# Kernel tuning notes

Measured on AMD Instinct MI355X. Metric: run time of the kernel, lower is better.

## Reference

```python
import jax, jax.numpy as jnp
import numpy as np

N_ENT = 500000
N_REL = 64
HID = 256
EMB = 128
E = 400000


def setup_inputs() -> dict:
    key = jax.random.key(0)
    k0, k1, k2, k3, k4 = jax.random.split(key, 5)
    s_in = 1.0 / np.sqrt(N_ENT + N_REL)
    s_h = 1.0 / np.sqrt(HID)
    return {
        "edge_index": jax.random.randint(k0, (2, E), 0, N_ENT),
        "edge_attr": jax.random.normal(k1, (E, N_REL), dtype=jnp.float32),
        "W1": jax.random.normal(k2, (N_ENT + N_REL, HID), dtype=jnp.float32) * s_in,
        "b1": jnp.zeros((HID,), dtype=jnp.float32),
        "W2": jax.random.normal(k3, (HID, HID), dtype=jnp.float32) * s_h,
        "b2": jnp.zeros((HID,), dtype=jnp.float32),
        "W3": jax.random.normal(k4, (HID, EMB), dtype=jnp.float32) * s_h,
        "b3": jnp.zeros((EMB,), dtype=jnp.float32),
    }


def reference(edge_index, edge_attr, W1, b1, W2, b2, W3, b3):
    # one_hot(edge_index, N_ENT) @ W1_ent is exactly a row gather from W1_ent.
    W1_ent = W1[:N_ENT]          # [N_ENT, HID]
    W1_rel = W1[N_ENT:]          # [N_REL, HID]
    rel_proj = edge_attr @ W1_rel            # [E, HID], shared by source/target
    h = W1_ent[edge_index] + rel_proj[None] + b1   # [2, E, HID]
    h = jax.nn.relu(h)
    h = jax.nn.relu(h @ W2 + b2)             # [2, E, HID]
    edge_emb = h @ W3 + b3                   # [2, E, EMB]
    return edge_emb
```

## Files before the change

kernel.cpp:

```cpp
#include <hip/hip_runtime.h>

#define N_ENT 500000
#define E_NUM 400000

typedef __attribute__((ext_vector_type(8))) short short8;
typedef __attribute__((ext_vector_type(4))) float f32x4;

static __device__ __forceinline__ unsigned short f2bf(float f) {
    unsigned u = __float_as_uint(f);
    u += 0x7fffu + ((u >> 16) & 1u);
    return (unsigned short)(u >> 16);
}
static __device__ __forceinline__ float bf2f(unsigned short s) {
    return __uint_as_float(((unsigned)s) << 16);
}

__global__ void pack_b_kernel(const float* __restrict__ src,
                              unsigned short* __restrict__ dst, int K, int N) {
    int p = blockIdx.x * blockDim.x + threadIdx.x;
    if (p >= K * N) return;
    int j = p & 7;
    int l = (p >> 3) & 63;
    int f = p >> 9;
    int nfr = N >> 4;
    int nb = f % nfr;
    int kb = f / nfr;
    int k = kb * 32 + ((l >> 4) << 3) + j;
    int n = nb * 16 + (l & 15);
    dst[p] = f2bf(src[(size_t)k * N + n]);
}

__device__ __forceinline__ int lds_off(int row, int colb) {
    return ((row << 9) + colb) ^ ((row & 7) << 4);
}

__global__ __launch_bounds__(256, 4) void fused2(
    const int* __restrict__ ei, const float* __restrict__ attr,
    const float* __restrict__ W1, const float* __restrict__ b1,
    const float* __restrict__ b2, const float* __restrict__ b3,
    const unsigned short* __restrict__ w1rp,
    const unsigned short* __restrict__ w2p,
    const unsigned short* __restrict__ w3p,
    float* __restrict__ out)
{
    __shared__ char hb[64 * 512];

    const int tid = threadIdx.x;
    const int l = tid & 63;
    const int wv = tid >> 6;
    const int lr = l & 15;
    const int lg = l >> 4;
    const int r0 = wv << 4;
    const int myrow = l >> 4;
    const int mycol = l & 15;

    const int bid = blockIdx.x;
    const int d = bid >= 6250 ? 1 : 0;
    const int e0 = (d ? bid - 6250 : bid) << 6;

    int ids[4];
    #pragma unroll
    for (int q = 0; q < 4; ++q)
        ids[q] = ei[d * E_NUM + e0 + r0 + (q << 2) + myrow];

    f32x4 g[4][4];
    #pragma unroll
    for (int q = 0; q < 4; ++q) {
        const float* gp = W1 + (size_t)ids[q] * 256 + (mycol << 2);
        #pragma unroll
        for (int k = 0; k < 4; ++k)
            g[q][k] = *(const f32x4*)(gp + (k << 6));
    }

    const float* ap = attr + (size_t)(e0 + r0 + lr) * 64 + (lg << 3);
    f32x4 ax[2][2];
    #pragma unroll
    for (int kb = 0; kb < 2; ++kb) {
        ax[kb][0] = *(const f32x4*)(ap + (kb << 5));
        ax[kb][1] = *(const f32x4*)(ap + (kb << 5) + 4);
    }

    #pragma unroll
    for (int q = 0; q < 4; ++q) {
        int row = r0 + (q << 2) + myrow;
        #pragma unroll
        for (int k = 0; k < 4; ++k) {
            unsigned lo = ((unsigned)f2bf(g[q][k][1]) << 16) | f2bf(g[q][k][0]);
            unsigned hi = ((unsigned)f2bf(g[q][k][3]) << 16) | f2bf(g[q][k][2]);
            int a = lds_off(row, (k << 7) + (mycol << 3));
            *(unsigned*)(hb + a) = lo;
            *(unsigned*)(hb + a + 4) = hi;
        }
    }

    const f32x4 zero = {0.f, 0.f, 0.f, 0.f};
    f32x4 acc[16];
    #pragma unroll
    for (int i = 0; i < 16; ++i) acc[i] = zero;
    #pragma unroll
    for (int kb = 0; kb < 2; ++kb) {
        short8 af;
        #pragma unroll
        for (int j = 0; j < 4; ++j) {
            af[j] = (short)f2bf(ax[kb][0][j]);
            af[j + 4] = (short)f2bf(ax[kb][1][j]);
        }
        #pragma unroll
        for (int cf = 0; cf < 16; ++cf)
            acc[cf] = __builtin_amdgcn_mfma_f32_16x16x32_bf16(
                af, ((const short8*)w1rp)[(size_t)(kb * 16 + cf) * 64 + l],
                acc[cf], 0, 0, 0);
    }

    #pragma unroll
    for (int reg = 0; reg < 4; ++reg) {
        int row = r0 + (lg << 2) + reg;
        #pragma unroll
        for (int cf = 0; cf < 16; ++cf) {
            int col = (cf << 4) + lr;
            int a = lds_off(row, col << 1);
            float v = acc[cf][reg] + bf2f(*(unsigned short*)(hb + a)) + b1[col];
            *(unsigned short*)(hb + a) = f2bf(fmaxf(v, 0.f));
        }
    }
    __syncthreads();

    f32x4 acc2[4][4];
    #pragma unroll
    for (int i = 0; i < 4; ++i)
        #pragma unroll
        for (int j = 0; j < 4; ++j) acc2[i][j] = zero;

    #pragma unroll 2
    for (int kb = 0; kb < 8; ++kb) {
        short8 a[4];
        #pragma unroll
        for (int mr = 0; mr < 4; ++mr)
            a[mr] = *(const short8*)(hb +
                lds_off(mr * 16 + lr, ((kb << 5) + (lg << 3)) << 1));
        #pragma unroll
        for (int mr = 0; mr < 4; ++mr)
            #pragma unroll
            for (int nf = 0; nf < 4; ++nf)
                acc2[mr][nf] = __builtin_amdgcn_mfma_f32_16x16x32_bf16(
                    a[mr],
                    ((const short8*)w2p)[(size_t)(kb * 16 + (wv << 2) + nf) * 64 + l],
                    acc2[mr][nf], 0, 0, 0);
    }
    __syncthreads();

    #pragma unroll
    for (int mr = 0; mr < 4; ++mr)
        #pragma unroll
        for (int reg = 0; reg < 4; ++reg) {
            int row = mr * 16 + (lg << 2) + reg;
            #pragma unroll
            for (int nf = 0; nf < 4; ++nf) {
                int col = (wv << 6) + (nf << 4) + lr;
                float v = fmaxf(acc2[mr][nf][reg] + b2[col], 0.f);
                *(unsigned short*)(hb + lds_off(row, col << 1)) = f2bf(v);
            }
        }
    __syncthreads();

    f32x4 acc3[4][2];
    #pragma unroll
    for (int i = 0; i < 4; ++i) { acc3[i][0] = zero; acc3[i][1] = zero; }

    #pragma unroll 2
    for (int kb = 0; kb < 8; ++kb) {
        short8 a[4];
        #pragma unroll
        for (int mr = 0; mr < 4; ++mr)
            a[mr] = *(const short8*)(hb +
                lds_off(mr * 16 + lr, ((kb << 5) + (lg << 3)) << 1));
        #pragma unroll
        for (int mr = 0; mr < 4; ++mr)
            #pragma unroll
            for (int nf = 0; nf < 2; ++nf)
                acc3[mr][nf] = __builtin_amdgcn_mfma_f32_16x16x32_bf16(
                    a[mr],
                    ((const short8*)w3p)[(size_t)(kb * 8 + (wv << 1) + nf) * 64 + l],
                    acc3[mr][nf], 0, 0, 0);
    }

    float* op = out + ((size_t)d * E_NUM + e0) * 128;
    #pragma unroll
    for (int mr = 0; mr < 4; ++mr)
        #pragma unroll
        for (int reg = 0; reg < 4; ++reg) {
            int row = mr * 16 + (lg << 2) + reg;
            #pragma unroll
            for (int nf = 0; nf < 2; ++nf) {
                int col = (wv << 5) + (nf << 4) + lr;
                op[(size_t)row * 128 + col] = acc3[mr][nf][reg] + b3[col];
            }
        }
}

extern "C" void kernel_launch(void* const* d_in, const int* in_sizes, int n_in,
                              void* d_out, int out_size, void* d_ws, size_t ws_size,
                              hipStream_t stream) {
    const int* ei     = (const int*)d_in[0];
    const float* attr = (const float*)d_in[1];
    const float* W1   = (const float*)d_in[2];
    const float* b1   = (const float*)d_in[3];
    const float* W2   = (const float*)d_in[4];
    const float* b2   = (const float*)d_in[5];
    const float* W3   = (const float*)d_in[6];
    const float* b3   = (const float*)d_in[7];
    float* out = (float*)d_out;
    const float* W1rel = W1 + (size_t)N_ENT * 256;

    unsigned short* w1rp = (unsigned short*)d_ws;
    unsigned short* w2p  = w1rp + 64 * 256;
    unsigned short* w3p  = w2p + 256 * 256;

    pack_b_kernel<<<(64 * 256) / 256, 256, 0, stream>>>(W1rel, w1rp, 64, 256);
    pack_b_kernel<<<(256 * 256) / 256, 256, 0, stream>>>(W2, w2p, 256, 256);
    pack_b_kernel<<<(256 * 128) / 256, 256, 0, stream>>>(W3, w3p, 256, 128);

    fused2<<<12500, 256, 0, stream>>>(ei, attr, W1, b1, b2, b3,
                                      w1rp, w2p, w3p, out);
}
```

Before: 424.0 us.

## Double block tile to 128 edges with 8 waves splitting output columns

Each block now handles 128 edges with 512 threads (8 waves), doubling LDS to 64KB. In layers 2 and 3 every wave covers all 128 rows and a narrower column slice, so each packed weight fragment fetched from global/L2 is reused across twice as many rows. The goal is to cut redundant weight traffic per edge. The cost is lower occupancy from the larger LDS footprint and launch bounds of (512,2), plus more LDS A-fragment reads per wave.

```diff
diff --git a/kernel.cpp b/kernel.cpp
--- a/kernel.cpp
+++ b/kernel.cpp
@@ -34,7 +34,7 @@
     return ((row << 9) + colb) ^ ((row & 7) << 4);
 }
 
-__global__ __launch_bounds__(256, 4) void fused2(
+__global__ __launch_bounds__(512, 2) void fused7(
     const int* __restrict__ ei, const float* __restrict__ attr,
     const float* __restrict__ W1, const float* __restrict__ b1,
     const float* __restrict__ b2, const float* __restrict__ b3,
@@ -43,7 +43,7 @@
     const unsigned short* __restrict__ w3p,
     float* __restrict__ out)
 {
-    __shared__ char hb[64 * 512];
+    __shared__ char hb[128 * 512];
 
     const int tid = threadIdx.x;
     const int l = tid & 63;
@@ -55,8 +55,8 @@
     const int mycol = l & 15;
 
     const int bid = blockIdx.x;
-    const int d = bid >= 6250 ? 1 : 0;
-    const int e0 = (d ? bid - 6250 : bid) << 6;
+    const int d = bid >= 3125 ? 1 : 0;
+    const int e0 = (d ? bid - 3125 : bid) << 7;
 
     int ids[4];
     #pragma unroll
@@ -125,76 +125,65 @@
     }
     __syncthreads();
 
-    f32x4 acc2[4][4];
-    #pragma unroll
-    for (int i = 0; i < 4; ++i)
-        #pragma unroll
-        for (int j = 0; j < 4; ++j) acc2[i][j] = zero;
+    f32x4 acc2[8][2];
+    #pragma unroll
+    for (int i = 0; i < 8; ++i) { acc2[i][0] = zero; acc2[i][1] = zero; }
 
     #pragma unroll 2
     for (int kb = 0; kb < 8; ++kb) {
-        short8 a[4];
-        #pragma unroll
-        for (int mr = 0; mr < 4; ++mr)
-            a[mr] = *(const short8*)(hb +
+        #pragma unroll
+        for (int mr = 0; mr < 8; ++mr) {
+            short8 a = *(const short8*)(hb +
                 lds_off(mr * 16 + lr, ((kb << 5) + (lg << 3)) << 1));
-        #pragma unroll
-        for (int mr = 0; mr < 4; ++mr)
-            #pragma unroll
-            for (int nf = 0; nf < 4; ++nf)
-                acc2[mr][nf] = __builtin_amdgcn_mfma_f32_16x16x32_bf16(
-                    a[mr],
-                    ((const short8*)w2p)[(size_t)(kb * 16 + (wv << 2) + nf) * 64 + l],
-                    acc2[mr][nf], 0, 0, 0);
-    }
-    __syncthreads();
-
-    #pragma unroll
-    for (int mr = 0; mr < 4; ++mr)
-        #pragma unroll
-        for (int reg = 0; reg < 4; ++reg) {
-            int row = mr * 16 + (lg << 2) + reg;
-            #pragma unroll
-            for (int nf = 0; nf < 4; ++nf) {
-                int col = (wv << 6) + (nf << 4) + lr;
-                float v = fmaxf(acc2[mr][nf][reg] + b2[col], 0.f);
-                *(unsigned short*)(hb + lds_off(row, col << 1)) = f2bf(v);
-            }
-        }
-    __syncthreads();
-
-    f32x4 acc3[4][2];
-    #pragma unroll
-    for (int i = 0; i < 4; ++i) { acc3[i][0] = zero; acc3[i][1] = zero; }
-
-    #pragma unroll 2
-    for (int kb = 0; kb < 8; ++kb) {
-        short8 a[4];
-        #pragma unroll
-        for (int mr = 0; mr < 4; ++mr)
-            a[mr] = *(const short8*)(hb +
-                lds_off(mr * 16 + lr, ((kb << 5) + (lg << 3)) << 1));
-        #pragma unroll
-        for (int mr = 0; mr < 4; ++mr)
             #pragma unroll
             for (int nf = 0; nf < 2; ++nf)
-                acc3[mr][nf] = __builtin_amdgcn_mfma_f32_16x16x32_bf16(
-                    a[mr],
-                    ((const short8*)w3p)[(size_t)(kb * 8 + (wv << 1) + nf) * 64 + l],
-                    acc3[mr][nf], 0, 0, 0);
-    }
-
-    float* op = out + ((size_t)d * E_NUM + e0) * 128;
-    #pragma unroll
-    for (int mr = 0; mr < 4; ++mr)
+                acc2[mr][nf] = __builtin_amdgcn_mfma_f32_16x16x32_bf16(
+                    a,
+                    ((const short8*)w2p)[(size_t)(kb * 16 + (wv << 1) + nf) * 64 + l],
+                    acc2[mr][nf], 0, 0, 0);
+        }
+    }
+    __syncthreads();
+
+    #pragma unroll
+    for (int mr = 0; mr < 8; ++mr)
         #pragma unroll
         for (int reg = 0; reg < 4; ++reg) {
             int row = mr * 16 + (lg << 2) + reg;
             #pragma unroll
             for (int nf = 0; nf < 2; ++nf) {
                 int col = (wv << 5) + (nf << 4) + lr;
-                op[(size_t)row * 128 + col] = acc3[mr][nf][reg] + b3[col];
+                float v = fmaxf(acc2[mr][nf][reg] + b2[col], 0.f);
+                *(unsigned short*)(hb + lds_off(row, col << 1)) = f2bf(v);
             }
+        }
+    __syncthreads();
+
+    f32x4 acc3[8];
+    #pragma unroll
+    for (int i = 0; i < 8; ++i) acc3[i] = zero;
+
+    #pragma unroll 2
+    for (int kb = 0; kb < 8; ++kb) {
+        #pragma unroll
+        for (int mr = 0; mr < 8; ++mr) {
+            short8 a = *(const short8*)(hb +
+                lds_off(mr * 16 + lr, ((kb << 5) + (lg << 3)) << 1));
+            acc3[mr] = __builtin_amdgcn_mfma_f32_16x16x32_bf16(
+                a,
+                ((const short8*)w3p)[(size_t)(kb * 8 + wv) * 64 + l],
+                acc3[mr], 0, 0, 0);
+        }
+    }
+
+    float* op = out + ((size_t)d * E_NUM + e0) * 128;
+    #pragma unroll
+    for (int mr = 0; mr < 8; ++mr)
+        #pragma unroll
+        for (int reg = 0; reg < 4; ++reg) {
+            int row = mr * 16 + (lg << 2) + reg;
+            int col = (wv << 4) + lr;
+            op[(size_t)row * 128 + col] = acc3[mr][reg] + b3[col];
         }
 }
 
@@ -220,6 +209,6 @@
     pack_b_kernel<<<(256 * 256) / 256, 256, 0, stream>>>(W2, w2p, 256, 256);
     pack_b_kernel<<<(256 * 128) / 256, 256, 0, stream>>>(W3, w3p, 256, 128);
 
-    fused2<<<12500, 256, 0, stream>>>(ei, attr, W1, b1, b2, b3,
-                                      w1rp, w2p, w3p, out);
-}
+    fused7<<<6250, 512, 0, stream>>>(ei, attr, W1, b1, b2, b3,
+                                     w1rp, w2p, w3p, out);
+}
```

Result: slower. 480.5 us (+13.3%).
